# Performance work log

Hardware: AMD Instinct MI355X
Metric: run time of the kernel (lower is better)

The kernel has to match this reference:

```python
import jax, jax.numpy as jnp
import numpy as np
import math

DIM = 1024
HEADS = 16
HEAD_DIM = DIM // HEADS
B, T = 4, 2048


def setup_inputs() -> dict:
    key = jax.random.key(0)
    ks = jax.random.split(key, 11)
    s = 1.0 / math.sqrt(DIM)
    return {
        "Q": jax.random.normal(ks[0], (B, T, DIM), jnp.float32),
        "K": jax.random.normal(ks[1], (B, T, DIM), jnp.float32),
        "V": jax.random.normal(ks[2], (B, T, DIM), jnp.float32),
        "Wq": jax.random.uniform(ks[3], (DIM, DIM), jnp.float32, -s, s),
        "bq": jax.random.uniform(ks[4], (DIM,), jnp.float32, -s, s),
        "Wk": jax.random.uniform(ks[5], (DIM, DIM), jnp.float32, -s, s),
        "bk": jax.random.uniform(ks[6], (DIM,), jnp.float32, -s, s),
        "Wv": jax.random.uniform(ks[7], (DIM, DIM), jnp.float32, -s, s),
        "bv": jax.random.uniform(ks[8], (DIM,), jnp.float32, -s, s),
        "Wo": jax.random.uniform(ks[9], (DIM, DIM), jnp.float32, -s, s),
        "bo": jax.random.uniform(ks[10], (DIM,), jnp.float32, -s, s),
    }


def reference(Q, K, V, Wq, bq, Wk, bk, Wv, bv, Wo, bo):
    # Linear projections (torch Linear: x @ W.T + b)
    q = Q @ Wq.T + bq  # [B,T,D]
    k = K @ Wk.T + bk
    v = V @ Wv.T + bv
    # split heads -> [B,H,T,hd]
    def split(x):
        return x.reshape(B, T, HEADS, HEAD_DIM).transpose(0, 2, 1, 3)
    qh, kh, vh = split(q), split(k), split(v)
    qh = qh / math.sqrt(HEAD_DIM)
    scores = jnp.einsum("bhtd,bhsd->bhts", qh, kh)  # [B,H,T,T]
    A = jax.nn.softmax(scores, axis=-1)  # dropout p=0 -> identity
    Oh = jnp.einsum("bhts,bhsd->bhtd", A, vh)  # [B,H,T,hd]
    O = Oh.transpose(0, 2, 1, 3).reshape(B, T, DIM)
    O = O @ Wo.T + bo
    weight = A.mean(axis=1)  # [B,T,T] averaged over heads
    return O, weight
```

## Files before the change

kernel.cpp:

```cpp
#include <hip/hip_runtime.h>
#include <stdint.h>

typedef __attribute__((ext_vector_type(8))) short bf16x8;
typedef __attribute__((ext_vector_type(4))) float f32x4;
typedef __attribute__((ext_vector_type(4))) unsigned int u32x4;

static constexpr int B_ = 4, T_ = 2048, D_ = 1024, H_ = 16, HD_ = 64;
static constexpr int BT_ = B_ * T_;
static constexpr float LOG2E_OVER_8 = 0.18033688011112042f;

#define DEV static __device__ __forceinline__

#define RAW_BAR() do { \
    __builtin_amdgcn_sched_barrier(0); \
    __builtin_amdgcn_s_barrier(); \
    __builtin_amdgcn_sched_barrier(0); \
} while (0)

DEV unsigned short f2bf(float f) {
    union { float f; uint32_t u; } v; v.f = f;
    uint32_t u = v.u;
    uint32_t r = (u + 0x7fffu + ((u >> 16) & 1u)) >> 16;
    return (unsigned short)r;
}

DEV uint32_t cvt_pk_bf16(float lo, float hi) {
    uint32_t r;
    asm("v_cvt_pk_bf16_f32 %0, %1, %2" : "=v"(r) : "v"(lo), "v"(hi));
    return r;
}

DEV float fexp2(float x) {
    float r;
    asm("v_exp_f32 %0, %1" : "=v"(r) : "v"(x));
    return r;
}

DEV void gll16(const void* g, void* l) {
    __builtin_amdgcn_global_load_lds(
        (const __attribute__((address_space(1))) void*)g,
        (__attribute__((address_space(3))) void*)l, 16, 0, 0);
}

__global__ __launch_bounds__(256)
void cast_fused(const float* __restrict__ q, const float* __restrict__ k, const float* __restrict__ v,
                const float* __restrict__ wq, const float* __restrict__ wk,
                const float* __restrict__ wv, const float* __restrict__ wo,
                unsigned short* __restrict__ oq, unsigned short* __restrict__ ok,
                unsigned short* __restrict__ ov, unsigned short* __restrict__ owq,
                unsigned short* __restrict__ owk, unsigned short* __restrict__ owv,
                unsigned short* __restrict__ owo) {
    const int y = blockIdx.y;
    const float* s; unsigned short* d; int n4;
    switch (y) {
        case 0: s = q;  d = oq;  n4 = BT_ * D_ / 4; break;
        case 1: s = k;  d = ok;  n4 = BT_ * D_ / 4; break;
        case 2: s = v;  d = ov;  n4 = BT_ * D_ / 4; break;
        case 3: s = wq; d = owq; n4 = D_ * D_ / 4; break;
        case 4: s = wk; d = owk; n4 = D_ * D_ / 4; break;
        case 5: s = wv; d = owv; n4 = D_ * D_ / 4; break;
        default: s = wo; d = owo; n4 = D_ * D_ / 4; break;
    }
    for (int i = blockIdx.x * blockDim.x + threadIdx.x; i < n4; i += gridDim.x * blockDim.x) {
        float4 vv = reinterpret_cast<const float4*>(s)[i];
        ushort4 o;
        o.x = f2bf(vv.x); o.y = f2bf(vv.y); o.z = f2bf(vv.z); o.w = f2bf(vv.w);
        reinterpret_cast<ushort4*>(d)[i] = o;
    }
}

__global__ __launch_bounds__(256, 3)
void gemm_qkv(const unsigned short* __restrict__ Aq, const unsigned short* __restrict__ Ak,
              const unsigned short* __restrict__ Av,
              const unsigned short* __restrict__ Wqb, const unsigned short* __restrict__ Wkb,
              const unsigned short* __restrict__ Wvb,
              const float* __restrict__ bq, const float* __restrict__ bk,
              const float* __restrict__ bv,
              unsigned short* __restrict__ oq, unsigned short* __restrict__ ok,
              unsigned short* __restrict__ vT) {
    constexpr int K = 1024, N = 1024, BK = 64;
    __shared__ unsigned short sA[128 * BK];
    __shared__ unsigned short sB[128 * BK];
    const int flat = blockIdx.x + (blockIdx.y << 3) + (blockIdx.z << 9);
    const int nbz = (flat & 7) * 192 + (flat >> 3);
    const int z = nbz >> 9;
    const int rem = nbz & 511;
    const int bm = rem >> 3, bn = rem & 7;

    const unsigned short* A = z == 0 ? Aq : z == 1 ? Ak : Av;
    const unsigned short* W = z == 0 ? Wqb : z == 1 ? Wkb : Wvb;
    const float* bias        = z == 0 ? bq : z == 1 ? bk : bv;
    const float oscale       = z == 0 ? LOG2E_OVER_8 : 1.0f;

    const int tid = threadIdx.x;
    const int lane = tid & 63, w = tid >> 6;
    const int c = lane & 15, g = lane >> 4;
    const int wr = w >> 1, wc = w & 1;
    const int rowA0 = bm * 128, rowB0 = bn * 128;

    f32x4 acc[4][4] = {};

    for (int k0 = 0; k0 < K; k0 += BK) {
        __syncthreads();
#pragma unroll
        for (int i = 0; i < 4; ++i) {
            int chunk = tid + i * 256;
            int row = chunk >> 3, c16 = chunk & 7;
            int sc16 = c16 ^ (row & 7);
            gll16(A + (size_t)(rowA0 + row) * K + k0 + sc16 * 8, (char*)sA + chunk * 16);
            gll16(W + (size_t)(rowB0 + row) * K + k0 + sc16 * 8, (char*)sB + chunk * 16);
        }
        __syncthreads();
#pragma unroll
        for (int kk = 0; kk < 2; ++kk) {
            bf16x8 af[4], bfr[4];
#pragma unroll
            for (int mf = 0; mf < 4; ++mf) {
                int row = wr * 64 + mf * 16 + c;
                int off = (row * 128 + kk * 64 + g * 16) ^ ((row & 7) << 4);
                af[mf] = *reinterpret_cast<const bf16x8*>((const char*)sA + off);
            }
#pragma unroll
            for (int nf = 0; nf < 4; ++nf) {
                int row = wc * 64 + nf * 16 + c;
                int off = (row * 128 + kk * 64 + g * 16) ^ ((row & 7) << 4);
                bfr[nf] = *reinterpret_cast<const bf16x8*>((const char*)sB + off);
            }
#pragma unroll
            for (int mf = 0; mf < 4; ++mf)
#pragma unroll
                for (int nf = 0; nf < 4; ++nf)
                    acc[mf][nf] = __builtin_amdgcn_mfma_f32_16x16x32_bf16(af[mf], bfr[nf], acc[mf][nf], 0, 0, 0);
        }
    }

    if (z == 2) {
#pragma unroll
        for (int mf = 0; mf < 4; ++mf) {
            int rowbase = rowA0 + wr * 64 + mf * 16 + g * 4;
            int bb = rowbase >> 11;
            int trow = rowbase & 2047;
            int blk = trow >> 6, off = trow & 63;
            int slot = (off & 32) | ((off & 8) << 1) | ((off & 4) << 1) | ((off & 16) >> 2);
#pragma unroll
            for (int nf = 0; nf < 4; ++nf) {
                int col = rowB0 + wc * 64 + nf * 16 + c;
                float bvv = bias[col];
                int hh = col >> 6, d = col & 63;
                ushort4 o;
                o.x = f2bf(acc[mf][nf][0] + bvv);
                o.y = f2bf(acc[mf][nf][1] + bvv);
                o.z = f2bf(acc[mf][nf][2] + bvv);
                o.w = f2bf(acc[mf][nf][3] + bvv);
                size_t addr = (((size_t)(bb * H_ + hh)) * HD_ + d) * T_ + blk * 64 + slot;
                *reinterpret_cast<ushort4*>(&vT[addr]) = o;
            }
        }
    } else {
        unsigned short* out = z == 0 ? oq : ok;
#pragma unroll
        for (int mf = 0; mf < 4; ++mf)
#pragma unroll
            for (int nf = 0; nf < 4; ++nf) {
                int col = rowB0 + wc * 64 + nf * 16 + c;
                float bvv = bias[col];
#pragma unroll
                for (int j = 0; j < 4; ++j) {
                    int row = rowA0 + wr * 64 + mf * 16 + g * 4 + j;
                    float v = (acc[mf][nf][j] + bvv) * oscale;
                    out[(size_t)row * N + col] = f2bf(v);
                }
            }
    }
}

__global__ __launch_bounds__(256, 3)
void gemm_o(const unsigned short* __restrict__ A, const unsigned short* __restrict__ W,
            const float* __restrict__ bias, float* __restrict__ out) {
    constexpr int K = 1024, N = 1024, BK = 64;
    __shared__ unsigned short sA[128 * BK];
    __shared__ unsigned short sB[128 * BK];
    const int tid = threadIdx.x;
    const int lane = tid & 63, w = tid >> 6;
    const int c = lane & 15, g = lane >> 4;
    const int flat = blockIdx.x + (blockIdx.y << 3);
    const int nbz = (flat & 7) * 64 + (flat >> 3);
    const int bm = nbz >> 3, bn = nbz & 7;
    const int wr = w >> 1, wc = w & 1;
    const int rowA0 = bm * 128, rowB0 = bn * 128;

    f32x4 acc[4][4] = {};

    for (int k0 = 0; k0 < K; k0 += BK) {
        __syncthreads();
#pragma unroll
        for (int i = 0; i < 4; ++i) {
            int chunk = tid + i * 256;
            int row = chunk >> 3, c16 = chunk & 7;
            int sc16 = c16 ^ (row & 7);
            gll16(A + (size_t)(rowA0 + row) * K + k0 + sc16 * 8, (char*)sA + chunk * 16);
            gll16(W + (size_t)(rowB0 + row) * K + k0 + sc16 * 8, (char*)sB + chunk * 16);
        }
        __syncthreads();
#pragma unroll
        for (int kk = 0; kk < 2; ++kk) {
            bf16x8 af[4], bfr[4];
#pragma unroll
            for (int mf = 0; mf < 4; ++mf) {
                int row = wr * 64 + mf * 16 + c;
                int off = (row * 128 + kk * 64 + g * 16) ^ ((row & 7) << 4);
                af[mf] = *reinterpret_cast<const bf16x8*>((const char*)sA + off);
            }
#pragma unroll
            for (int nf = 0; nf < 4; ++nf) {
                int row = wc * 64 + nf * 16 + c;
                int off = (row * 128 + kk * 64 + g * 16) ^ ((row & 7) << 4);
                bfr[nf] = *reinterpret_cast<const bf16x8*>((const char*)sB + off);
            }
#pragma unroll
            for (int mf = 0; mf < 4; ++mf)
#pragma unroll
                for (int nf = 0; nf < 4; ++nf)
                    acc[mf][nf] = __builtin_amdgcn_mfma_f32_16x16x32_bf16(af[mf], bfr[nf], acc[mf][nf], 0, 0, 0);
        }
    }
#pragma unroll
    for (int mf = 0; mf < 4; ++mf)
#pragma unroll
        for (int nf = 0; nf < 4; ++nf) {
            int col = rowB0 + wc * 64 + nf * 16 + c;
            float bvv = bias[col];
#pragma unroll
            for (int j = 0; j < 4; ++j) {
                int row = rowA0 + wr * 64 + mf * 16 + g * 4 + j;
                out[(size_t)row * N + col] = acc[mf][nf][j] + bvv;
            }
        }
}

__global__ __launch_bounds__(256, 4)
void flash_kernel(const unsigned short* __restrict__ qbf,
                  const unsigned short* __restrict__ kbf,
                  const unsigned short* __restrict__ vT,
                  unsigned short* __restrict__ ohbf,
                  float* __restrict__ madjOut) {
    __shared__ unsigned short sK[2][64 * 64];
    __shared__ unsigned short sV[2][64 * 64];
    const int tid = threadIdx.x, lane = tid & 63, w = tid >> 6;
    const int c = lane & 15, g = lane >> 4;
    const int nb = (blockIdx.x & 7) * 128 + (blockIdx.x >> 3);
    const int t0 = (nb & 15) * 128, h = (nb >> 4) & 15, b = nb >> 8;

    bf16x8 qf[2][2];
#pragma unroll
    for (int u = 0; u < 2; ++u) {
        const size_t qbase = ((size_t)(b * T_) + t0 + w * 32 + u * 16 + c) * D_ + h * HD_;
        qf[u][0] = *reinterpret_cast<const bf16x8*>(qbf + qbase + g * 8);
        qf[u][1] = *reinterpret_cast<const bf16x8*>(qbf + qbase + 32 + g * 8);
    }

    const unsigned short one_bf = 0x3F80;
    const bf16x8 ones = { (short)one_bf, (short)one_bf, (short)one_bf, (short)one_bf,
                          (short)one_bf, (short)one_bf, (short)one_bf, (short)one_bf };

    f32x4 acc[2][4] = {};
    f32x4 acc_l[2] = {};

    const unsigned short* kRow = kbf + (size_t)b * T_ * D_ + h * HD_;
    const unsigned short* vRow = vT + ((size_t)(b * H_ + h)) * HD_ * T_;

    auto stage = [&](int buf, int s0) {
#pragma unroll
        for (int i = 0; i < 2; ++i) {
            int chunk = tid + i * 256;
            int row = chunk >> 3, c16 = chunk & 7;
            int sc16 = c16 ^ (row & 7);
            gll16(kRow + (size_t)(s0 + row) * D_ + sc16 * 8, (char*)sK[buf] + chunk * 16);
            gll16(vRow + (size_t)row * T_ + s0 + sc16 * 8, (char*)sV[buf] + chunk * 16);
        }
    };

    stage(0, 0);
    constexpr int NT = T_ / 64;

    for (int it = 0; it < NT; ++it) {
        const int cur = it & 1;
        if (it + 1 < NT) {
            stage(cur ^ 1, (it + 1) * 64);
            asm volatile("s_waitcnt vmcnt(4)" ::: "memory");
        } else {
            asm volatile("s_waitcnt vmcnt(0)" ::: "memory");
        }
        RAW_BAR();

        const char* sKc = (const char*)sK[cur];
        const char* sVc = (const char*)sV[cur];

        f32x4 sc[2][4] = {};
        __builtin_amdgcn_s_setprio(1);
#pragma unroll
        for (int kk = 0; kk < 2; ++kk)
#pragma unroll
            for (int nf = 0; nf < 4; ++nf) {
                int row = nf * 16 + c;
                int off = (row * 128 + kk * 64 + g * 16) ^ ((row & 7) << 4);
                bf16x8 kf = *reinterpret_cast<const bf16x8*>(sKc + off);
                sc[0][nf] = __builtin_amdgcn_mfma_f32_16x16x32_bf16(kf, qf[0][kk], sc[0][nf], 0, 0, 0);
                sc[1][nf] = __builtin_amdgcn_mfma_f32_16x16x32_bf16(kf, qf[1][kk], sc[1][nf], 0, 0, 0);
            }
        __builtin_amdgcn_s_setprio(0);

        u32x4 pkw[2][2];
#pragma unroll
        for (int u = 0; u < 2; ++u) {
#pragma unroll
            for (int nf = 0; nf < 4; ++nf)
#pragma unroll
                for (int j = 0; j < 4; ++j)
                    sc[u][nf][j] = fexp2(sc[u][nf][j]);
#pragma unroll
            for (int kk = 0; kk < 2; ++kk) {
                u32x4 pw;
                pw.x = cvt_pk_bf16(sc[u][2 * kk][0], sc[u][2 * kk][1]);
                pw.y = cvt_pk_bf16(sc[u][2 * kk][2], sc[u][2 * kk][3]);
                pw.z = cvt_pk_bf16(sc[u][2 * kk + 1][0], sc[u][2 * kk + 1][1]);
                pw.w = cvt_pk_bf16(sc[u][2 * kk + 1][2], sc[u][2 * kk + 1][3]);
                pkw[u][kk] = pw;
            }
        }

        __builtin_amdgcn_s_setprio(1);
#pragma unroll
        for (int kk = 0; kk < 2; ++kk) {
            bf16x8 pa0 = __builtin_bit_cast(bf16x8, pkw[0][kk]);
            bf16x8 pa1 = __builtin_bit_cast(bf16x8, pkw[1][kk]);
#pragma unroll
            for (int nf = 0; nf < 4; ++nf) {
                int row = nf * 16 + c;
                int voff = (row * 128 + kk * 64 + g * 16) ^ ((row & 7) << 4);
                bf16x8 vf = *reinterpret_cast<const bf16x8*>(sVc + voff);
                acc[0][nf] = __builtin_amdgcn_mfma_f32_16x16x32_bf16(pa0, vf, acc[0][nf], 0, 0, 0);
                acc[1][nf] = __builtin_amdgcn_mfma_f32_16x16x32_bf16(pa1, vf, acc[1][nf], 0, 0, 0);
            }
            acc_l[0] = __builtin_amdgcn_mfma_f32_16x16x32_bf16(pa0, ones, acc_l[0], 0, 0, 0);
            acc_l[1] = __builtin_amdgcn_mfma_f32_16x16x32_bf16(pa1, ones, acc_l[1], 0, 0, 0);
        }
        __builtin_amdgcn_s_setprio(0);
        RAW_BAR();
    }

#pragma unroll
    for (int u = 0; u < 2; ++u) {
#pragma unroll
        for (int j = 0; j < 4; ++j) {
            float inv = 1.f / acc_l[u][j];
            int trow = t0 + w * 32 + u * 16 + g * 4 + j;
#pragma unroll
            for (int nf = 0; nf < 4; ++nf)
                ohbf[((size_t)(b * T_) + trow) * D_ + h * HD_ + nf * 16 + c] = f2bf(acc[u][nf][j] * inv);
            if (c == 0)
                madjOut[((size_t)(b * H_ + h)) * T_ + trow] = 4.0f + __log2f(acc_l[u][j]);
        }
    }
}

__global__ __launch_bounds__(256, 3)
void weight_kernel(const unsigned short* __restrict__ qbf,
                   const unsigned short* __restrict__ kbf,
                   const float* __restrict__ madjIn,
                   float* __restrict__ wout) {
    __shared__ unsigned short sQ[2][64 * 64];
    __shared__ unsigned short sK2[2][128 * 64];
    __shared__ float sMadj[16][64];
    const int tid = threadIdx.x, lane = tid & 63, w = tid >> 6;
    const int c = lane & 15, g = lane >> 4;
    const int nb = (blockIdx.x & 7) * 256 + (blockIdx.x >> 3);
    const int s0 = (nb & 15) * 128, t0 = ((nb >> 4) & 31) * 64, b = nb >> 9;

    float wacc[4][2][4] = {};

    auto stageW = [&](int buf, int h) {
#pragma unroll
        for (int i = 0; i < 2; ++i) {
            int chunk = tid + i * 256;
            int row = chunk >> 3, c16 = chunk & 7;
            int sc16 = c16 ^ (row & 7);
            gll16(qbf + ((size_t)(b * T_) + t0 + row) * D_ + h * HD_ + sc16 * 8,
                  (char*)sQ[buf] + chunk * 16);
        }
#pragma unroll
        for (int i = 0; i < 4; ++i) {
            int chunk = tid + i * 256;
            int row = chunk >> 3, c16 = chunk & 7;
            int sc16 = c16 ^ (row & 7);
            gll16(kbf + ((size_t)(b * T_) + s0 + row) * D_ + h * HD_ + sc16 * 8,
                  (char*)sK2[buf] + chunk * 16);
        }
    };

    {
        int hh = tid >> 4, tq = tid & 15;
        float4 mv = *reinterpret_cast<const float4*>(
            &madjIn[((size_t)(b * H_ + hh)) * T_ + t0 + tq * 4]);
        *reinterpret_cast<float4*>(&sMadj[hh][tq * 4]) = mv;
    }
    __syncthreads();

    stageW(0, 0);

    for (int h = 0; h < H_; ++h) {
        const int cur = h & 1;
        if (h + 1 < H_) {
            stageW(cur ^ 1, h + 1);
            asm volatile("s_waitcnt vmcnt(6)" ::: "memory");
        } else {
            asm volatile("s_waitcnt vmcnt(0)" ::: "memory");
        }
        RAW_BAR();

        const char* sQc = (const char*)sQ[cur];
        const char* sKc = (const char*)sK2[cur];

        f32x4 sc[4][2];
#pragma unroll
        for (int mf = 0; mf < 4; ++mf) {
            f32x4 mrow = *reinterpret_cast<const f32x4*>(&sMadj[h][mf * 16 + g * 4]);
#pragma unroll
            for (int j = 0; j < 4; ++j) {
                sc[mf][0][j] = -mrow[j];
                sc[mf][1][j] = -mrow[j];
            }
        }

        __builtin_amdgcn_s_setprio(1);
#pragma unroll
        for (int kk = 0; kk < 2; ++kk) {
            bf16x8 af[4], bfr[2];
#pragma unroll
            for (int mf = 0; mf < 4; ++mf) {
                int row = mf * 16 + c;
                int off = (row * 128 + kk * 64 + g * 16) ^ ((row & 7) << 4);
                af[mf] = *reinterpret_cast<const bf16x8*>(sQc + off);
            }
#pragma unroll
            for (int nf = 0; nf < 2; ++nf) {
                int row = w * 32 + nf * 16 + c;
                int off = (row * 128 + kk * 64 + g * 16) ^ ((row & 7) << 4);
                bfr[nf] = *reinterpret_cast<const bf16x8*>(sKc + off);
            }
#pragma unroll
            for (int mf = 0; mf < 4; ++mf)
#pragma unroll
                for (int nf = 0; nf < 2; ++nf)
                    sc[mf][nf] = __builtin_amdgcn_mfma_f32_16x16x32_bf16(af[mf], bfr[nf], sc[mf][nf], 0, 0, 0);
        }
        __builtin_amdgcn_s_setprio(0);
#pragma unroll
        for (int mf = 0; mf < 4; ++mf)
#pragma unroll
            for (int nf = 0; nf < 2; ++nf)
#pragma unroll
                for (int j = 0; j < 4; ++j)
                    wacc[mf][nf][j] += fexp2(sc[mf][nf][j]);
        RAW_BAR();
    }
#pragma unroll
    for (int mf = 0; mf < 4; ++mf)
#pragma unroll
        for (int j = 0; j < 4; ++j) {
            int trow = t0 + mf * 16 + g * 4 + j;
#pragma unroll
            for (int nf = 0; nf < 2; ++nf) {
                int col = s0 + w * 32 + nf * 16 + c;
                wout[((size_t)b * T_ + trow) * (size_t)T_ + col] = wacc[mf][nf][j];
            }
        }
}

extern "C" void kernel_launch(void* const* d_in, const int* in_sizes, int n_in,
                              void* d_out, int out_size, void* d_ws, size_t ws_size,
                              hipStream_t stream) {
    const float* Q  = (const float*)d_in[0];
    const float* K  = (const float*)d_in[1];
    const float* V  = (const float*)d_in[2];
    const float* Wq = (const float*)d_in[3];
    const float* bq = (const float*)d_in[4];
    const float* Wk = (const float*)d_in[5];
    const float* bk = (const float*)d_in[6];
    const float* Wv = (const float*)d_in[7];
    const float* bv = (const float*)d_in[8];
    const float* Wo = (const float*)d_in[9];
    const float* bo = (const float*)d_in[10];

    char* ws = (char*)d_ws;
    const size_t MB = 1u << 20;
    unsigned short* Wqb = (unsigned short*)(ws);
    unsigned short* Wkb = Wqb + 1024 * 1024;
    unsigned short* Wvb = Wkb + 1024 * 1024;
    unsigned short* Wob = Wvb + 1024 * 1024;
    unsigned short* Qc  = (unsigned short*)(ws + 8 * MB);
    unsigned short* Kc  = (unsigned short*)(ws + 24 * MB);
    unsigned short* Vc  = (unsigned short*)(ws + 40 * MB);
    unsigned short* qb  = (unsigned short*)(ws + 56 * MB);
    unsigned short* kb  = (unsigned short*)(ws + 72 * MB);
    unsigned short* vT  = (unsigned short*)(ws + 88 * MB);
    unsigned short* ohb = Kc;
    float* mArr = (float*)(ws + 104 * MB);

    cast_fused<<<dim3(1024, 7), 256, 0, stream>>>(Q, K, V, Wq, Wk, Wv, Wo,
                                                  Qc, Kc, Vc, Wqb, Wkb, Wvb, Wob);

    gemm_qkv<<<dim3(8, 64, 3), 256, 0, stream>>>(Qc, Kc, Vc, Wqb, Wkb, Wvb,
                                                 bq, bk, bv, qb, kb, vT);

    flash_kernel<<<1024, 256, 0, stream>>>(qb, kb, vT, ohb, mArr);

    float* Oout = (float*)d_out;
    float* Wout = Oout + (size_t)BT_ * D_;
    gemm_o<<<dim3(8, 64), 256, 0, stream>>>(ohb, Wob, bo, Oout);
    weight_kernel<<<2048, 256, 0, stream>>>(qb, kb, mArr, Wout);
}
```

Measured before the change: 256.3 us.

## Split flash kernel work across eight waves with 16 query rows each

The flash attention kernel now launches 512 threads per block, and each of the eight waves handles 16 query rows instead of two 16-row slabs per wave with four waves. Per-wave registers for Q fragments, accumulators and scores are halved, and the K/V staging becomes one 16-byte load per thread with a matching wait count. The aim is more waves in flight to hide the exp and LDS latency. In exchange, each K/V fragment read from LDS is reused by only one MFMA instead of two, which doubles LDS read traffic per unit of compute, and the block barriers now synchronise twice as many waves.

```diff
diff --git a/kernel.cpp b/kernel.cpp
--- a/kernel.cpp
+++ b/kernel.cpp
@@ -238,7 +238,7 @@
         }
 }
 
-__global__ __launch_bounds__(256, 4)
+__global__ __launch_bounds__(512, 8)
 void flash_kernel(const unsigned short* __restrict__ qbf,
                   const unsigned short* __restrict__ kbf,
                   const unsigned short* __restrict__ vT,
@@ -251,33 +251,27 @@
     const int nb = (blockIdx.x & 7) * 128 + (blockIdx.x >> 3);
     const int t0 = (nb & 15) * 128, h = (nb >> 4) & 15, b = nb >> 8;
 
-    bf16x8 qf[2][2];
-#pragma unroll
-    for (int u = 0; u < 2; ++u) {
-        const size_t qbase = ((size_t)(b * T_) + t0 + w * 32 + u * 16 + c) * D_ + h * HD_;
-        qf[u][0] = *reinterpret_cast<const bf16x8*>(qbf + qbase + g * 8);
-        qf[u][1] = *reinterpret_cast<const bf16x8*>(qbf + qbase + 32 + g * 8);
+    bf16x8 qf[2];
+    {
+        const size_t qbase = ((size_t)(b * T_) + t0 + w * 16 + c) * D_ + h * HD_;
+        qf[0] = *reinterpret_cast<const bf16x8*>(qbf + qbase + g * 8);
+        qf[1] = *reinterpret_cast<const bf16x8*>(qbf + qbase + 32 + g * 8);
     }
 
     const unsigned short one_bf = 0x3F80;
     const bf16x8 ones = { (short)one_bf, (short)one_bf, (short)one_bf, (short)one_bf,
                           (short)one_bf, (short)one_bf, (short)one_bf, (short)one_bf };
 
-    f32x4 acc[2][4] = {};
-    f32x4 acc_l[2] = {};
+    f32x4 acc[4] = {};
+    f32x4 acc_l = {};
 
     const unsigned short* kRow = kbf + (size_t)b * T_ * D_ + h * HD_;
     const unsigned short* vRow = vT + ((size_t)(b * H_ + h)) * HD_ * T_;
 
+    const int srow = tid >> 3, sc16 = (tid & 7) ^ (srow & 7);
     auto stage = [&](int buf, int s0) {
-#pragma unroll
-        for (int i = 0; i < 2; ++i) {
-            int chunk = tid + i * 256;
-            int row = chunk >> 3, c16 = chunk & 7;
-            int sc16 = c16 ^ (row & 7);
-            gll16(kRow + (size_t)(s0 + row) * D_ + sc16 * 8, (char*)sK[buf] + chunk * 16);
-            gll16(vRow + (size_t)row * T_ + s0 + sc16 * 8, (char*)sV[buf] + chunk * 16);
-        }
+        gll16(kRow + (size_t)(s0 + srow) * D_ + sc16 * 8, (char*)sK[buf] + tid * 16);
+        gll16(vRow + (size_t)srow * T_ + s0 + sc16 * 8, (char*)sV[buf] + tid * 16);
     };
 
     stage(0, 0);
@@ -287,7 +281,7 @@
         const int cur = it & 1;
         if (it + 1 < NT) {
             stage(cur ^ 1, (it + 1) * 64);
-            asm volatile("s_waitcnt vmcnt(4)" ::: "memory");
+            asm volatile("s_waitcnt vmcnt(2)" ::: "memory");
         } else {
             asm volatile("s_waitcnt vmcnt(0)" ::: "memory");
         }
@@ -296,7 +290,7 @@
         const char* sKc = (const char*)sK[cur];
         const char* sVc = (const char*)sV[cur];
 
-        f32x4 sc[2][4] = {};
+        f32x4 sc[4] = {};
         __builtin_amdgcn_s_setprio(1);
 #pragma unroll
         for (int kk = 0; kk < 2; ++kk)
@@ -305,62 +299,53 @@
                 int row = nf * 16 + c;
                 int off = (row * 128 + kk * 64 + g * 16) ^ ((row & 7) << 4);
                 bf16x8 kf = *reinterpret_cast<const bf16x8*>(sKc + off);
-                sc[0][nf] = __builtin_amdgcn_mfma_f32_16x16x32_bf16(kf, qf[0][kk], sc[0][nf], 0, 0, 0);
-                sc[1][nf] = __builtin_amdgcn_mfma_f32_16x16x32_bf16(kf, qf[1][kk], sc[1][nf], 0, 0, 0);
+                sc[nf] = __builtin_amdgcn_mfma_f32_16x16x32_bf16(kf, qf[kk], sc[nf], 0, 0, 0);
             }
         __builtin_amdgcn_s_setprio(0);
 
-        u32x4 pkw[2][2];
-#pragma unroll
-        for (int u = 0; u < 2; ++u) {
-#pragma unroll
-            for (int nf = 0; nf < 4; ++nf)
-#pragma unroll
-                for (int j = 0; j < 4; ++j)
-                    sc[u][nf][j] = fexp2(sc[u][nf][j]);
-#pragma unroll
-            for (int kk = 0; kk < 2; ++kk) {
-                u32x4 pw;
-                pw.x = cvt_pk_bf16(sc[u][2 * kk][0], sc[u][2 * kk][1]);
-                pw.y = cvt_pk_bf16(sc[u][2 * kk][2], sc[u][2 * kk][3]);
-                pw.z = cvt_pk_bf16(sc[u][2 * kk + 1][0], sc[u][2 * kk + 1][1]);
-                pw.w = cvt_pk_bf16(sc[u][2 * kk + 1][2], sc[u][2 * kk + 1][3]);
-                pkw[u][kk] = pw;
-            }
+#pragma unroll
+        for (int nf = 0; nf < 4; ++nf)
+#pragma unroll
+            for (int j = 0; j < 4; ++j)
+                sc[nf][j] = fexp2(sc[nf][j]);
+
+        u32x4 pkw[2];
+#pragma unroll
+        for (int kk = 0; kk < 2; ++kk) {
+            u32x4 pw;
+            pw.x = cvt_pk_bf16(sc[2 * kk][0], sc[2 * kk][1]);
+            pw.y = cvt_pk_bf16(sc[2 * kk][2], sc[2 * kk][3]);
+            pw.z = cvt_pk_bf16(sc[2 * kk + 1][0], sc[2 * kk + 1][1]);
+            pw.w = cvt_pk_bf16(sc[2 * kk + 1][2], sc[2 * kk + 1][3]);
+            pkw[kk] = pw;
         }
 
         __builtin_amdgcn_s_setprio(1);
 #pragma unroll
         for (int kk = 0; kk < 2; ++kk) {
-            bf16x8 pa0 = __builtin_bit_cast(bf16x8, pkw[0][kk]);
-            bf16x8 pa1 = __builtin_bit_cast(bf16x8, pkw[1][kk]);
+            bf16x8 pa = __builtin_bit_cast(bf16x8, pkw[kk]);
 #pragma unroll
             for (int nf = 0; nf < 4; ++nf) {
                 int row = nf * 16 + c;
                 int voff = (row * 128 + kk * 64 + g * 16) ^ ((row & 7) << 4);
                 bf16x8 vf = *reinterpret_cast<const bf16x8*>(sVc + voff);
-                acc[0][nf] = __builtin_amdgcn_mfma_f32_16x16x32_bf16(pa0, vf, acc[0][nf], 0, 0, 0);
-                acc[1][nf] = __builtin_amdgcn_mfma_f32_16x16x32_bf16(pa1, vf, acc[1][nf], 0, 0, 0);
-            }
-            acc_l[0] = __builtin_amdgcn_mfma_f32_16x16x32_bf16(pa0, ones, acc_l[0], 0, 0, 0);
-            acc_l[1] = __builtin_amdgcn_mfma_f32_16x16x32_bf16(pa1, ones, acc_l[1], 0, 0, 0);
+                acc[nf] = __builtin_amdgcn_mfma_f32_16x16x32_bf16(pa, vf, acc[nf], 0, 0, 0);
+            }
+            acc_l = __builtin_amdgcn_mfma_f32_16x16x32_bf16(pa, ones, acc_l, 0, 0, 0);
         }
         __builtin_amdgcn_s_setprio(0);
         RAW_BAR();
     }
 
 #pragma unroll
-    for (int u = 0; u < 2; ++u) {
-#pragma unroll
-        for (int j = 0; j < 4; ++j) {
-            float inv = 1.f / acc_l[u][j];
-            int trow = t0 + w * 32 + u * 16 + g * 4 + j;
-#pragma unroll
-            for (int nf = 0; nf < 4; ++nf)
-                ohbf[((size_t)(b * T_) + trow) * D_ + h * HD_ + nf * 16 + c] = f2bf(acc[u][nf][j] * inv);
-            if (c == 0)
-                madjOut[((size_t)(b * H_ + h)) * T_ + trow] = 4.0f + __log2f(acc_l[u][j]);
-        }
+    for (int j = 0; j < 4; ++j) {
+        float inv = 1.f / acc_l[j];
+        int trow = t0 + w * 16 + g * 4 + j;
+#pragma unroll
+        for (int nf = 0; nf < 4; ++nf)
+            ohbf[((size_t)(b * T_) + trow) * D_ + h * HD_ + nf * 16 + c] = f2bf(acc[nf][j] * inv);
+        if (c == 0)
+            madjOut[((size_t)(b * H_ + h)) * T_ + trow] = 4.0f + __log2f(acc_l[j]);
     }
 }
 
@@ -513,7 +498,7 @@
     gemm_qkv<<<dim3(8, 64, 3), 256, 0, stream>>>(Qc, Kc, Vc, Wqb, Wkb, Wvb,
                                                  bq, bk, bv, qb, kb, vT);
 
-    flash_kernel<<<1024, 256, 0, stream>>>(qb, kb, vT, ohb, mArr);
+    flash_kernel<<<1024, 512, 0, stream>>>(qb, kb, vT, ohb, mArr);
 
     float* Oout = (float*)d_out;
     float* Wout = Oout + (size_t)BT_ * D_;
```

Result: slower. 266.8 us (+4.1%).
